# Optimization experiments

Hardware: AMD Instinct MI355X
Metric: run time of the kernel (lower is better)

## Reference

```python
import jax, jax.numpy as jnp
import numpy as np

BN_EPS = 1e-5


def setup_inputs() -> dict:
    key = jax.random.key(0)
    ks = jax.random.split(key, 11)
    B, C, Ci, D, H, W = 2, 256, 128, 8, 32, 32
    s = 0.02  # weight init scale
    return {
        "x": jax.random.normal(ks[0], (B, C, D, H, W), dtype=jnp.float32),
        "Wt": jax.random.normal(ks[1], (Ci, C), dtype=jnp.float32) * s,
        "bt": jax.random.normal(ks[2], (Ci,), dtype=jnp.float32) * s,
        "Wp": jax.random.normal(ks[3], (Ci, C), dtype=jnp.float32) * s,
        "bp": jax.random.normal(ks[4], (Ci,), dtype=jnp.float32) * s,
        "Wg": jax.random.normal(ks[5], (Ci, C), dtype=jnp.float32) * s,
        "bg": jax.random.normal(ks[6], (Ci,), dtype=jnp.float32) * s,
        "Ww": jax.random.normal(ks[7], (C, Ci), dtype=jnp.float32) * s,
        "bw": jax.random.normal(ks[8], (C,), dtype=jnp.float32) * s,
        "gamma": jax.random.normal(ks[9], (C,), dtype=jnp.float32),
        "beta": jax.random.normal(ks[10], (C,), dtype=jnp.float32),
    }


def reference(x, Wt, bt, Wp, bp, Wg, bg, Ww, bw, gamma, beta):
    # x: [B, C, D, H, W]; 1x1x1 Conv3d == per-position channel GEMM.
    B, C, D, H, W = x.shape
    xf = x.reshape(B, C, -1)  # [B, C, N], N = D*H*W

    theta = jnp.einsum('oc,bcn->bno', Wt, xf) + bt          # [B, N, Ci]
    phi = jnp.einsum('oc,bcn->bon', Wp, xf) + bp[None, :, None]  # [B, Ci, N]
    g = jnp.einsum('oc,bcn->bno', Wg, xf) + bg              # [B, N, Ci]

    # Unscaled, unmasked full self-attention over all N spatial positions.
    f = jnp.einsum('bnc,bcm->bnm', theta, phi)              # [B, N, N]
    a = jax.nn.softmax(f, axis=-1)
    y = jnp.einsum('bnm,bmc->bcn', a, g)                    # [B, Ci, N]

    # Output projection W: conv1x1 then BatchNorm3d (training-mode batch stats).
    wy = jnp.einsum('oc,bcn->bon', Ww, y) + bw[None, :, None]  # [B, C, N]
    mean = jnp.mean(wy, axis=(0, 2), keepdims=True)
    var = jnp.var(wy, axis=(0, 2), keepdims=True)
    wy_bn = (wy - mean) * jax.lax.rsqrt(var + BN_EPS)
    wy_bn = wy_bn * gamma[None, :, None] + beta[None, :, None]

    return wy_bn.reshape(B, C, D, H, W) + x
```

## Files before the change

kernel.cpp:

```cpp
#include <hip/hip_runtime.h>
#include <cstdint>
#include <cstddef>


typedef unsigned short u16;
typedef __bf16 bf16x8 __attribute__((ext_vector_type(8)));
typedef float f32x4 __attribute__((ext_vector_type(4)));
typedef float f32x16 __attribute__((ext_vector_type(16)));
typedef unsigned short u16x8 __attribute__((ext_vector_type(8)));

#define B_ 2
#define C_ 256
#define CI_ 128
#define N_ 8192
#define KVB 64

static __device__ __forceinline__ u16 f2bf(float f){
  unsigned u = __builtin_bit_cast(unsigned, f);
  unsigned r = (u + 0x7FFFu + ((u>>16)&1u)) >> 16;
  return (u16)r;
}
static __device__ __forceinline__ float bf2f(u16 v){
  unsigned u = ((unsigned)v) << 16;
  return __builtin_bit_cast(float, u);
}
static __device__ __forceinline__ float fexp2(float x){
  return __builtin_amdgcn_exp2f(x);
}
static __device__ __forceinline__ f32x4 f4zero(){
  f32x4 v; v[0]=0.f; v[1]=0.f; v[2]=0.f; v[3]=0.f; return v;
}
static __device__ __forceinline__ f32x16 f16zero(){
  f32x16 v;
#pragma unroll
  for (int i=0;i<16;i++) v[i]=0.f;
  return v;
}
static __device__ __forceinline__ f32x4 mfma16(bf16x8 a, bf16x8 b, f32x4 c){
  return __builtin_amdgcn_mfma_f32_16x16x32_bf16(a, b, c, 0, 0, 0);
}
static __device__ __forceinline__ f32x16 mfma32(bf16x8 a, bf16x8 b, f32x16 c){
  return __builtin_amdgcn_mfma_f32_32x32x16_bf16(a, b, c, 0, 0, 0);
}
static __device__ __forceinline__ unsigned cvtpk(float lo, float hi){
  unsigned r;
  asm("v_cvt_pk_bf16_f32 %0, %1, %2" : "=v"(r) : "v"(lo), "v"(hi));
  return r;
}
static __device__ __forceinline__ void plswap(unsigned &a, unsigned &b){
  asm volatile("v_permlane32_swap_b32 %0, %1" : "+v"(a), "+v"(b));
}

#define LOG2E 1.4426950408889634f

__global__ __launch_bounds__(256) void k1_proj(const float* __restrict__ x,
     const float* __restrict__ Wt, const float* __restrict__ Wp,
     const float* __restrict__ Wg, const float* __restrict__ bt,
     const float* __restrict__ bp, const float* __restrict__ bg,
     u16* __restrict__ theta, u16* __restrict__ kproj, u16* __restrict__ gT,
     float* __restrict__ stats){
  __shared__ u16 At[64*264];
  __shared__ u16 Wt_[32*264];
  __shared__ u16 gbuf[32*72];
  int tid = threadIdx.x;
  int b  = blockIdx.x >> 7;
  int nb = (blockIdx.x & 127) * 64;
  int w = tid >> 6, lane = tid & 63;
  int l15 = lane & 15, kg = lane >> 4;

  if (blockIdx.x == 0){
    stats[tid] = 0.f; stats[256 + tid] = 0.f;
  }

  {
    int cp = tid & 127, nh = tid >> 7;
    int c0 = cp*2;
    const float* src0 = x + ((size_t)(b*C_ + c0))*N_ + nb + nh*32;
    const float* src1 = src0 + N_;
#pragma unroll
    for (int j=0;j<8;j++){
      f32x4 a = *(const f32x4*)(src0 + j*4);
      f32x4 c = *(const f32x4*)(src1 + j*4);
#pragma unroll
      for (int q=0;q<4;q++){
        unsigned pk = (unsigned)f2bf(a[q]) | ((unsigned)f2bf(c[q])<<16);
        *(unsigned*)&At[(nh*32 + j*4 + q)*264 + c0] = pk;
      }
    }
  }
  __syncthreads();

  bf16x8 afr[8];
#pragma unroll
  for (int kc=0;kc<8;kc++)
    afr[kc] = *(const bf16x8*)&At[(w*16+l15)*264 + kc*32 + kg*8];

  for (int och = 0; och < 12; och++){
    {
      int o8 = tid>>3, cp8 = tid&7;
      const float* wsel = (och<4) ? (Wt + ((size_t)(och*32 + o8))*256)
                        : (och<8) ? (Wp + ((size_t)((och-4)*32 + o8))*256)
                                  : (Wg + ((size_t)((och-8)*32 + o8))*256);
      float scl = (och<4) ? LOG2E : 1.f;
#pragma unroll
      for (int j=0;j<4;j++){
        f32x4 w0 = *(const f32x4*)(wsel + cp8*8 + j*64);
        f32x4 w1 = *(const f32x4*)(wsel + cp8*8 + j*64 + 4);
        u16 tmp[8];
#pragma unroll
        for (int q=0;q<4;q++){ tmp[q] = f2bf(w0[q]*scl); tmp[4+q] = f2bf(w1[q]*scl); }
        *(u16x8*)&Wt_[o8*264 + cp8*8 + j*64] = *(const u16x8*)tmp;
      }
    }
    __syncthreads();

    f32x4 acc0 = f4zero(), acc1 = f4zero();
#pragma unroll
    for (int kc=0;kc<8;kc++){
      bf16x8 b0 = *(const bf16x8*)&Wt_[(l15)*264 + kc*32 + kg*8];
      bf16x8 b1 = *(const bf16x8*)&Wt_[(16+l15)*264 + kc*32 + kg*8];
      acc0 = mfma16(afr[kc], b0, acc0);
      acc1 = mfma16(afr[kc], b1, acc1);
    }

    if (och < 8){
      u16* dst = (och < 4) ? theta : kproj;
      int oo = (och & 3) * 32;
#pragma unroll
      for (int of=0;of<2;of++){
        int o = oo + of*16 + l15;
        float bias = (och<4) ? bt[och*32 + of*16 + l15] * LOG2E
                             : bp[(och-4)*32 + of*16 + l15];
        f32x4 acc = of ? acc1 : acc0;
#pragma unroll
        for (int i=0;i<4;i++){
          int n = nb + w*16 + kg*4 + i;
          dst[((size_t)b*N_ + n)*CI_ + o] = f2bf(acc[i] + bias);
        }
      }
      __syncthreads();
    } else {
#pragma unroll
      for (int of=0;of<2;of++){
        int o = of*16 + l15;
        float bias = bg[(och-8)*32 + of*16 + l15];
        f32x4 acc = of ? acc1 : acc0;
#pragma unroll
        for (int i=0;i<4;i++){
          int r = w*16 + kg*4 + i;
          gbuf[o*72 + r] = f2bf(acc[i] + bias);
        }
      }
      __syncthreads();
      {
        int o = tid>>3, np = tid&7;
        int og = (och-8)*32 + o;
        u16x8 v = *(const u16x8*)&gbuf[o*72 + np*8];
        *(u16x8*)(gT + ((size_t)b*CI_ + og)*N_ + nb + np*8) = v;
      }
      __syncthreads();
    }
  }
}

__global__ __launch_bounds__(512, 2) void k2_attn(const u16* __restrict__ theta,
      const u16* __restrict__ kproj, const u16* __restrict__ gT,
      u16* __restrict__ pO, float* __restrict__ pM, float* __restrict__ pL){
  constexpr int CHUNK_N = 2048;
  constexpr int NTI = CHUNK_N / KVB;
  __shared__ char smem[81920];
  int tid = threadIdx.x;
  int bid = blockIdx.x;
  int combo = bid & 7;
  int b = combo & 1;
  int chunk = combo >> 1;
  int qblk = bid >> 3;
  int n0 = chunk * CHUNK_N;
  int w = tid >> 6, lane = tid & 63;
  int l31 = lane & 31, hi = lane >> 5;
  int qg = qblk*256 + w*32 + l31;

  char* kb_cur = smem;
  char* kb_nxt = smem + 16384;
  char* vb_cur = smem + 32768;
  char* vb_nxt = smem + 49152;
  char* vb_prev = smem + 65536;

  bf16x8 qf[8];
  {
    const u16* qsrc = theta + ((size_t)b*N_ + qg)*CI_ + hi*8;
#pragma unroll
    for (int cc=0; cc<8; cc++) qf[cc] = *(const bf16x8*)(qsrc + cc*16);
  }

  int krow_s = tid >> 3, kpart = tid & 7;
  int vrow_s = tid >> 2, vpart = tid & 3;
  const u16* ksrc = kproj + ((size_t)b*N_ + n0 + krow_s)*CI_ + kpart*16;
  const u16* vsrc = gT + ((size_t)b*CI_ + vrow_s)*N_ + n0 + vpart*16;
  int kw_off[2], vw_off[2];
#pragma unroll
  for (int j=0;j<2;j++){
    int cb = kpart*32 + j*16;
    kw_off[j] = krow_s*256 + (cb ^ ((krow_s&15)<<4));
    int kb = vpart*32 + j*16;
    vw_off[j] = vrow_s*128 + (kb ^ ((vrow_s&7)<<4));
  }
  int kswz = (l31&15)<<4;
  int vswz = (l31&7)<<4;
  int kro[8], vro[4];
#pragma unroll
  for (int cc=0;cc<8;cc++) kro[cc] = l31*256 + ((cc*32 + hi*16) ^ kswz);
#pragma unroll
  for (int ks=0;ks<4;ks++) vro[ks] = l31*128 + ((ks*32 + hi*16) ^ vswz);

#pragma unroll
  for (int j=0;j<2;j++){
    *(u16x8*)(kb_cur + kw_off[j]) = *(const u16x8*)(ksrc + j*8);
    *(u16x8*)(vb_cur + vw_off[j]) = *(const u16x8*)(vsrc + j*8);
  }
  __syncthreads();

  f32x16 oacc[4];
#pragma unroll
  for (int i=0;i<4;i++) oacc[i] = f16zero();
  float mrun = -1e30f, lrun = 0.f;
  f32x16 sA0, sB0, sA1, sB1;

#define K2_ROT() { char* _t = vb_prev; vb_prev = vb_cur; vb_cur = vb_nxt; vb_nxt = _t; \
                   char* _k = kb_cur; kb_cur = kb_nxt; kb_nxt = _k; }

#define K2_MAX(CA, CB) { float t8[8]; \
    _Pragma("unroll") \
    for (int i=0;i<8;i++) t8[i] = fmaxf(fmaxf(CA[i], CA[i+8]), fmaxf(CB[i], CB[i+8])); \
    float mx = fmaxf(fmaxf(fmaxf(t8[0],t8[4]),fmaxf(t8[1],t8[5])), \
                     fmaxf(fmaxf(t8[2],t8[6]),fmaxf(t8[3],t8[7]))); \
    mx = fmaxf(mx, __shfl_xor(mx, 32)); \
    if (__any(mx > mrun + 12.f)){ \
      float mnew = fmaxf(mrun, mx); \
      float sc = fexp2(mrun - mnew); \
      lrun *= sc; \
      _Pragma("unroll") \
      for (int i=0;i<4;i++){ _Pragma("unroll") for (int r=0;r<16;r++) oacc[i][r] *= sc; } \
      mrun = mnew; } }

#define K2_EXP(PA, PB, pA, pB) \
    float pA[16], pB[16]; \
    _Pragma("unroll") \
    for (int r=0;r<16;r++){ pA[r] = fexp2(PA[r]-mrun); pB[r] = fexp2(PB[r]-mrun); } \
    { float s8[8]; \
      _Pragma("unroll") \
      for (int i=0;i<8;i++) s8[i] = (pA[i]+pA[i+8]) + (pB[i]+pB[i+8]); \
      float ps = ((s8[0]+s8[4])+(s8[1]+s8[5])) + ((s8[2]+s8[6])+(s8[3]+s8[7])); \
      ps += __shfl_xor(ps, 32); lrun += ps; }

#define K2_PV(pA, pB) \
    __builtin_amdgcn_s_setprio(1); \
    _Pragma("unroll") \
    for (int ks=0; ks<4; ks++){ \
      const float* P = (ks<2) ? pA : pB; \
      int r0 = (ks&1)*8; \
      unsigned a0 = cvtpk(P[r0+0], P[r0+1]); \
      unsigned b0 = cvtpk(P[r0+4], P[r0+5]); \
      unsigned a1 = cvtpk(P[r0+2], P[r0+3]); \
      unsigned b1 = cvtpk(P[r0+6], P[r0+7]); \
      plswap(a0, b0); plswap(a1, b1); \
      union { unsigned u[4]; bf16x8 v; } pb; \
      pb.u[0]=a0; pb.u[1]=a1; pb.u[2]=b0; pb.u[3]=b1; \
      _Pragma("unroll") \
      for (int c2=0; c2<4; c2++){ \
        bf16x8 vf = *(const bf16x8*)(vb_prev + c2*4096 + vro[ks]); \
        oacc[c2] = mfma32(vf, pb.v, oacc[c2]); \
      } \
    } \
    __builtin_amdgcn_s_setprio(0);

#define K2_QKT(CA, CB) \
    CA = f16zero(); CB = f16zero(); \
    __builtin_amdgcn_s_setprio(1); \
    _Pragma("unroll") \
    for (int cc=0; cc<8; cc++){ \
      bf16x8 kf0 = *(const bf16x8*)(kb_cur + kro[cc]); \
      bf16x8 kf1 = *(const bf16x8*)(kb_cur + 8192 + kro[cc]); \
      CA = mfma32(kf0, qf[cc], CA); \
      CB = mfma32(kf1, qf[cc], CB); \
    } \
    __builtin_amdgcn_s_setprio(0);

#define K2_LOADS(T) \
    int tn = ((T)+1 < NTI) ? ((T)+1) : (NTI-1); \
    u16x8 kst0 = *(const u16x8*)(ksrc + (size_t)tn*KVB*CI_); \
    u16x8 kst1 = *(const u16x8*)(ksrc + (size_t)tn*KVB*CI_ + 8); \
    u16x8 vst0 = *(const u16x8*)(vsrc + tn*KVB); \
    u16x8 vst1 = *(const u16x8*)(vsrc + tn*KVB + 8);

#define K2_WRITES() \
    *(u16x8*)(kb_nxt + kw_off[0]) = kst0; *(u16x8*)(kb_nxt + kw_off[1]) = kst1; \
    *(u16x8*)(vb_nxt + vw_off[0]) = vst0; *(u16x8*)(vb_nxt + vw_off[1]) = vst1;

#define K2_ITER(T, CA, CB, PA, PB) { \
    K2_LOADS(T) \
    K2_QKT(CA, CB) \
    K2_EXP(PA, PB, pA_, pB_) \
    K2_WRITES() \
    K2_PV(pA_, pB_) \
    K2_MAX(CA, CB) \
    __syncthreads(); \
    K2_ROT() }

  {
    K2_LOADS(0)
    K2_QKT(sA0, sB0)
    K2_WRITES()
    K2_MAX(sA0, sB0)
    __syncthreads();
    K2_ROT()
  }
  for (int t = 1; t < NTI-1; t += 2){
    K2_ITER(t,   sA1, sB1, sA0, sB0)
    K2_ITER(t+1, sA0, sB0, sA1, sB1)
  }
  K2_ITER(NTI-1, sA1, sB1, sA0, sB0)

  {
    K2_EXP(sA1, sB1, pA_, pB_)
    K2_PV(pA_, pB_)
  }
  __syncthreads();

  char* region = smem + w*8192;
#pragma unroll
  for (int c2=0;c2<4;c2++)
#pragma unroll
    for (int r=0;r<16;r++){
      int c = c2*32 + (r&3) + 8*(r>>2) + 4*hi;
      *(u16*)(region + l31*256 + ((c*2) ^ vswz)) = f2bf(oacc[c2][r]);
    }
  __syncthreads();
  {
    int ql = lane >> 1, half = lane & 1;
    int qg2 = qblk*256 + w*32 + ql;
    u16* dst = pO + ((size_t)(chunk*2 + b)*N_ + qg2)*CI_ + half*64;
    int rswz = (ql&7)<<4;
#pragma unroll
    for (int j=0;j<8;j++){
      u16x8 v2 = *(const u16x8*)(region + ql*256 + ((half*128 + j*16) ^ rswz));
      *(u16x8*)(dst + j*8) = v2;
    }
  }
  if (hi == 0){
    pM[(size_t)(chunk*2 + b)*N_ + qg] = mrun;
    pL[(size_t)(chunk*2 + b)*N_ + qg] = lrun;
  }
}

__global__ __launch_bounds__(256) void k3_wy(const u16* __restrict__ pO,
    const float* __restrict__ pM, const float* __restrict__ pL,
    const float* __restrict__ Ww, const float* __restrict__ bw,
    u16* __restrict__ wy, float* __restrict__ stats){
  __shared__ u16 Yt[64*136];
  __shared__ u16 Wt_[64*136];
  __shared__ float wyb[64*72];
  int tid = threadIdx.x;
  int b  = blockIdx.x >> 7;
  int nb = (blockIdx.x & 127) * 64;
  int w = tid>>6, lane = tid&63;
  int l15 = lane&15, kg = lane>>4;

  {
    int n = tid>>2, cp = tid&3;
    size_t q = (size_t)nb + n;
    float m[4], l[4];
#pragma unroll
    for (int ch=0; ch<4; ch++){
      m[ch] = pM[(size_t)(ch*2+b)*N_ + q];
      l[ch] = pL[(size_t)(ch*2+b)*N_ + q];
    }
    float M = fmaxf(fmaxf(m[0],m[1]), fmaxf(m[2],m[3]));
    float wts[4]; float L = 0.f;
#pragma unroll
    for (int ch=0; ch<4; ch++){ wts[ch] = exp2f(m[ch]-M); L += wts[ch]*l[ch]; }
    float inv = 1.f/L;
#pragma unroll
    for (int j=0;j<4;j++){
      int c0 = cp*32 + j*8;
      float acc[8];
#pragma unroll
      for (int i=0;i<8;i++) acc[i]=0.f;
#pragma unroll
      for (int ch=0; ch<4; ch++){
        u16x8 v = *(const u16x8*)(pO + ((size_t)(ch*2+b)*N_ + q)*CI_ + c0);
#pragma unroll
        for (int i=0;i<8;i++) acc[i] += wts[ch]*bf2f(v[i]);
      }
#pragma unroll
      for (int i=0;i<4;i++){
        unsigned pk = (unsigned)f2bf(acc[2*i]*inv) | ((unsigned)f2bf(acc[2*i+1]*inv)<<16);
        *(unsigned*)&Yt[n*136 + c0 + 2*i] = pk;
      }
    }
  }
  __syncthreads();

  bf16x8 afr[4];
#pragma unroll
  for (int kc=0;kc<4;kc++)
    afr[kc] = *(const bf16x8*)&Yt[(w*16+l15)*136 + kc*32 + kg*8];

  for (int oc=0; oc<4; oc++){
    {
      int o = tid>>2, cp = tid&3;
      const float* src = Ww + ((size_t)(oc*64 + o))*CI_ + cp*32;
#pragma unroll
      for (int j=0;j<4;j++){
        f32x4 w0 = *(const f32x4*)(src + j*8);
        f32x4 w1 = *(const f32x4*)(src + j*8 + 4);
        u16 tmp[8];
#pragma unroll
        for (int q2=0;q2<4;q2++){ tmp[q2] = f2bf(w0[q2]); tmp[4+q2] = f2bf(w1[q2]); }
        *(u16x8*)&Wt_[o*136 + cp*32 + j*8] = *(const u16x8*)tmp;
      }
    }
    __syncthreads();

    f32x4 acc[4];
#pragma unroll
    for (int of=0;of<4;of++) acc[of] = f4zero();
#pragma unroll
    for (int kc=0;kc<4;kc++){
#pragma unroll
      for (int of=0;of<4;of++){
        bf16x8 bfr = *(const bf16x8*)&Wt_[(of*16+l15)*136 + kc*32 + kg*8];
        acc[of] = mfma16(afr[kc], bfr, acc[of]);
      }
    }
#pragma unroll
    for (int of=0;of<4;of++){
#pragma unroll
      for (int i=0;i<4;i++)
        wyb[(of*16+l15)*72 + w*16 + kg*4 + i] = acc[of][i];
    }
    __syncthreads();
    {
      int o = tid>>2, np = tid&3;
      int og = oc*64 + o;
      float bias = bw[og];
      float sm = 0.f, sq = 0.f;
      u16* dst = wy + ((size_t)b*C_ + og)*N_ + nb + np*16;
      u16 buf[16];
#pragma unroll
      for (int j=0;j<4;j++){
#pragma unroll
        for (int q2=0;q2<4;q2++){
          float t2 = wyb[o*72 + np*16 + j*4 + q2] + bias;
          buf[j*4+q2] = f2bf(t2); sm += t2; sq += t2*t2;
        }
      }
      *(u16x8*)dst = *(const u16x8*)&buf[0];
      *(u16x8*)(dst+8) = *(const u16x8*)&buf[8];
      sm += __shfl_xor(sm, 1); sm += __shfl_xor(sm, 2);
      sq += __shfl_xor(sq, 1); sq += __shfl_xor(sq, 2);
      if ((tid&3)==0){
        atomicAdd(&stats[og], sm);
        atomicAdd(&stats[256+og], sq);
      }
    }
    __syncthreads();
  }
}

__global__ __launch_bounds__(256) void k4_bn(const u16* __restrict__ wy,
    const float* __restrict__ x, const float* __restrict__ stats,
    const float* __restrict__ gamma, const float* __restrict__ beta,
    float* __restrict__ out){
  size_t base = ((size_t)blockIdx.x)*2048 + (size_t)threadIdx.x*8;
  int o = (int)((base >> 13) & 255);
  const float invn = 1.f/16384.f;
  float mean = stats[o]*invn;
  float var  = stats[256+o]*invn - mean*mean;
  float rs = rsqrtf(var + 1e-5f);
  float g = gamma[o]*rs;
  float bb = beta[o];
  u16x8 a = *(const u16x8*)(wy + base);
  f32x4 x0 = *(const f32x4*)(x + base);
  f32x4 x1 = *(const f32x4*)(x + base + 4);
  f32x4 r0, r1;
#pragma unroll
  for (int q=0;q<4;q++){
    r0[q] = (bf2f(a[q])-mean)*g + bb + x0[q];
    r1[q] = (bf2f(a[4+q])-mean)*g + bb + x1[q];
  }
  *(f32x4*)(out + base)     = r0;
  *(f32x4*)(out + base + 4) = r1;
}

extern "C" void kernel_launch(void* const* d_in, const int* in_sizes, int n_in,
                              void* d_out, int out_size, void* d_ws, size_t ws_size,
                              hipStream_t stream){
  const float* x     = (const float*)d_in[0];
  const float* Wt    = (const float*)d_in[1];
  const float* bt    = (const float*)d_in[2];
  const float* Wp    = (const float*)d_in[3];
  const float* bp    = (const float*)d_in[4];
  const float* Wg    = (const float*)d_in[5];
  const float* bg    = (const float*)d_in[6];
  const float* Ww    = (const float*)d_in[7];
  const float* bw    = (const float*)d_in[8];
  const float* gamma = (const float*)d_in[9];
  const float* beta  = (const float*)d_in[10];

  char* ws = (char*)d_ws;
  u16*   theta = (u16*)(ws + 0);
  u16*   kproj = (u16*)(ws + 4194304);
  u16*   gT    = (u16*)(ws + 8388608);
  u16*   pO    = (u16*)(ws + 12582912);
  float* pM    = (float*)(ws + 29360128);
  float* pL    = (float*)(ws + 29622272);
  u16*   wy    = (u16*)(ws + 29884416);
  float* stats = (float*)(ws + 38273024);
  float* out   = (float*)d_out;

  k1_proj<<<256, 256, 0, stream>>>(x, Wt, Wp, Wg, bt, bp, bg, theta, kproj, gT, stats);
  k2_attn<<<256, 512, 0, stream>>>(theta, kproj, gT, pO, pM, pL);
  k3_wy<<<256, 256, 0, stream>>>(pO, pM, pL, Ww, bw, wy, stats);
  k4_bn<<<2048, 256, 0, stream>>>(wy, x, stats, gamma, beta, out);
}
```

Measured before the change: 131.1 us.

## Restructure attention KV pipeline to two-tile stages with one barrier per pair

Replaces the software-pipelined loop, which overlapped QK^T of tile t with PV of tile t-1 across triple-buffered V and double-buffered K, with a simpler scheme. Each stage now loads two KV tiles into a double-buffered half of LDS and processes both tiles sequentially, with one barrier per pair. This halves the number of __syncthreads and prefetches twice as much data per stage. It gives up the QK/PV interleaving within an iteration and raises LDS use from 80KB to 128KB, which can limit blocks per CU.

```diff
diff --git a/kernel.cpp b/kernel.cpp
--- a/kernel.cpp
+++ b/kernel.cpp
@@ -168,7 +168,10 @@
       u16* __restrict__ pO, float* __restrict__ pM, float* __restrict__ pL){
   constexpr int CHUNK_N = 2048;
   constexpr int NTI = CHUNK_N / KVB;
-  __shared__ char smem[81920];
+  constexpr int NS  = NTI/2;
+  __shared__ char smem[131072];
+  char* kbase = smem;
+  char* vbase = smem + 65536;
   int tid = threadIdx.x;
   int bid = blockIdx.x;
   int combo = bid & 7;
@@ -180,12 +183,6 @@
   int l31 = lane & 31, hi = lane >> 5;
   int qg = qblk*256 + w*32 + l31;
 
-  char* kb_cur = smem;
-  char* kb_nxt = smem + 16384;
-  char* vb_cur = smem + 32768;
-  char* vb_nxt = smem + 49152;
-  char* vb_prev = smem + 65536;
-
   bf16x8 qf[8];
   {
     const u16* qsrc = theta + ((size_t)b*N_ + qg)*CI_ + hi*8;
@@ -215,8 +212,10 @@
 
 #pragma unroll
   for (int j=0;j<2;j++){
-    *(u16x8*)(kb_cur + kw_off[j]) = *(const u16x8*)(ksrc + j*8);
-    *(u16x8*)(vb_cur + vw_off[j]) = *(const u16x8*)(vsrc + j*8);
+    *(u16x8*)(kbase + kw_off[j])         = *(const u16x8*)(ksrc + j*8);
+    *(u16x8*)(kbase + 16384 + kw_off[j]) = *(const u16x8*)(ksrc + (size_t)KVB*CI_ + j*8);
+    *(u16x8*)(vbase + vw_off[j])         = *(const u16x8*)(vsrc + j*8);
+    *(u16x8*)(vbase + 16384 + vw_off[j]) = *(const u16x8*)(vsrc + KVB + j*8);
   }
   __syncthreads();
 
@@ -224,14 +223,21 @@
 #pragma unroll
   for (int i=0;i<4;i++) oacc[i] = f16zero();
   float mrun = -1e30f, lrun = 0.f;
-  f32x16 sA0, sB0, sA1, sB1;
-
-#define K2_ROT() { char* _t = vb_prev; vb_prev = vb_cur; vb_cur = vb_nxt; vb_nxt = _t; \
-                   char* _k = kb_cur; kb_cur = kb_nxt; kb_nxt = _k; }
-
-#define K2_MAX(CA, CB) { float t8[8]; \
+
+#define K2_TILE(KB, VB) { \
+    f32x16 sA = f16zero(), sB = f16zero(); \
+    __builtin_amdgcn_s_setprio(1); \
     _Pragma("unroll") \
-    for (int i=0;i<8;i++) t8[i] = fmaxf(fmaxf(CA[i], CA[i+8]), fmaxf(CB[i], CB[i+8])); \
+    for (int cc=0; cc<8; cc++){ \
+      bf16x8 kf0 = *(const bf16x8*)((KB) + kro[cc]); \
+      bf16x8 kf1 = *(const bf16x8*)((KB) + 8192 + kro[cc]); \
+      sA = mfma32(kf0, qf[cc], sA); \
+      sB = mfma32(kf1, qf[cc], sB); \
+    } \
+    __builtin_amdgcn_s_setprio(0); \
+    float t8[8]; \
+    _Pragma("unroll") \
+    for (int i=0;i<8;i++) t8[i] = fmaxf(fmaxf(sA[i], sA[i+8]), fmaxf(sB[i], sB[i+8])); \
     float mx = fmaxf(fmaxf(fmaxf(t8[0],t8[4]),fmaxf(t8[1],t8[5])), \
                      fmaxf(fmaxf(t8[2],t8[6]),fmaxf(t8[3],t8[7]))); \
     mx = fmaxf(mx, __shfl_xor(mx, 32)); \
@@ -241,19 +247,15 @@
       lrun *= sc; \
       _Pragma("unroll") \
       for (int i=0;i<4;i++){ _Pragma("unroll") for (int r=0;r<16;r++) oacc[i][r] *= sc; } \
-      mrun = mnew; } }
-
-#define K2_EXP(PA, PB, pA, pB) \
+      mrun = mnew; } \
     float pA[16], pB[16]; \
     _Pragma("unroll") \
-    for (int r=0;r<16;r++){ pA[r] = fexp2(PA[r]-mrun); pB[r] = fexp2(PB[r]-mrun); } \
+    for (int r=0;r<16;r++){ pA[r] = fexp2(sA[r]-mrun); pB[r] = fexp2(sB[r]-mrun); } \
     { float s8[8]; \
       _Pragma("unroll") \
       for (int i=0;i<8;i++) s8[i] = (pA[i]+pA[i+8]) + (pB[i]+pB[i+8]); \
       float ps = ((s8[0]+s8[4])+(s8[1]+s8[5])) + ((s8[2]+s8[6])+(s8[3]+s8[7])); \
-      ps += __shfl_xor(ps, 32); lrun += ps; }
-
-#define K2_PV(pA, pB) \
+      ps += __shfl_xor(ps, 32); lrun += ps; } \
     __builtin_amdgcn_s_setprio(1); \
     _Pragma("unroll") \
     for (int ks=0; ks<4; ks++){ \
@@ -268,64 +270,49 @@
       pb.u[0]=a0; pb.u[1]=a1; pb.u[2]=b0; pb.u[3]=b1; \
       _Pragma("unroll") \
       for (int c2=0; c2<4; c2++){ \
-        bf16x8 vf = *(const bf16x8*)(vb_prev + c2*4096 + vro[ks]); \
+        bf16x8 vf = *(const bf16x8*)((VB) + c2*4096 + vro[ks]); \
         oacc[c2] = mfma32(vf, pb.v, oacc[c2]); \
       } \
     } \
-    __builtin_amdgcn_s_setprio(0);
-
-#define K2_QKT(CA, CB) \
-    CA = f16zero(); CB = f16zero(); \
-    __builtin_amdgcn_s_setprio(1); \
-    _Pragma("unroll") \
-    for (int cc=0; cc<8; cc++){ \
-      bf16x8 kf0 = *(const bf16x8*)(kb_cur + kro[cc]); \
-      bf16x8 kf1 = *(const bf16x8*)(kb_cur + 8192 + kro[cc]); \
-      CA = mfma32(kf0, qf[cc], CA); \
-      CB = mfma32(kf1, qf[cc], CB); \
-    } \
-    __builtin_amdgcn_s_setprio(0);
-
-#define K2_LOADS(T) \
-    int tn = ((T)+1 < NTI) ? ((T)+1) : (NTI-1); \
-    u16x8 kst0 = *(const u16x8*)(ksrc + (size_t)tn*KVB*CI_); \
-    u16x8 kst1 = *(const u16x8*)(ksrc + (size_t)tn*KVB*CI_ + 8); \
-    u16x8 vst0 = *(const u16x8*)(vsrc + tn*KVB); \
-    u16x8 vst1 = *(const u16x8*)(vsrc + tn*KVB + 8);
-
-#define K2_WRITES() \
-    *(u16x8*)(kb_nxt + kw_off[0]) = kst0; *(u16x8*)(kb_nxt + kw_off[1]) = kst1; \
-    *(u16x8*)(vb_nxt + vw_off[0]) = vst0; *(u16x8*)(vb_nxt + vw_off[1]) = vst1;
-
-#define K2_ITER(T, CA, CB, PA, PB) { \
-    K2_LOADS(T) \
-    K2_QKT(CA, CB) \
-    K2_EXP(PA, PB, pA_, pB_) \
-    K2_WRITES() \
-    K2_PV(pA_, pB_) \
-    K2_MAX(CA, CB) \
-    __syncthreads(); \
-    K2_ROT() }
-
-  {
-    K2_LOADS(0)
-    K2_QKT(sA0, sB0)
-    K2_WRITES()
-    K2_MAX(sA0, sB0)
+    __builtin_amdgcn_s_setprio(0); }
+
+  for (int s = 0; s < NS; s++){
+    int H = s & 1;
+    char* kh = kbase + H*32768;
+    char* vh = vbase + H*32768;
+    u16x8 kst[4], vst[4];
+    bool pf = (s+1 < NS);
+    if (pf){
+      const u16* ks = ksrc + (size_t)(2*s+2)*KVB*CI_;
+      const u16* vs = vsrc + (2*s+2)*KVB;
+      kst[0] = *(const u16x8*)(ks);
+      kst[1] = *(const u16x8*)(ks + 8);
+      kst[2] = *(const u16x8*)(ks + (size_t)KVB*CI_);
+      kst[3] = *(const u16x8*)(ks + (size_t)KVB*CI_ + 8);
+      vst[0] = *(const u16x8*)(vs);
+      vst[1] = *(const u16x8*)(vs + 8);
+      vst[2] = *(const u16x8*)(vs + KVB);
+      vst[3] = *(const u16x8*)(vs + KVB + 8);
+    }
+
+    K2_TILE(kh, vh)
+
+    if (pf){
+      char* kd = kbase + (H^1)*32768;
+      char* vd = vbase + (H^1)*32768;
+#pragma unroll
+      for (int j=0;j<2;j++){
+        *(u16x8*)(kd + kw_off[j])         = kst[j];
+        *(u16x8*)(kd + 16384 + kw_off[j]) = kst[2+j];
+        *(u16x8*)(vd + vw_off[j])         = vst[j];
+        *(u16x8*)(vd + 16384 + vw_off[j]) = vst[2+j];
+      }
+    }
+
+    K2_TILE(kh + 16384, vh + 16384)
+
     __syncthreads();
-    K2_ROT()
-  }
-  for (int t = 1; t < NTI-1; t += 2){
-    K2_ITER(t,   sA1, sB1, sA0, sB0)
-    K2_ITER(t+1, sA0, sB0, sA1, sB1)
-  }
-  K2_ITER(NTI-1, sA1, sB1, sA0, sB0)
-
-  {
-    K2_EXP(sA1, sB1, pA_, pB_)
-    K2_PV(pA_, pB_)
-  }
-  __syncthreads();
+  }
 
   char* region = smem + w*8192;
 #pragma unroll
```

New measurement: 132.6 us. No clear change (+1.2%).
